# Kernel optimization log

Measured on AMD Instinct MI355X. Metric: run time of the kernel, lower is better.

The kernel has to match this reference:

```python
import jax, jax.numpy as jnp
import numpy as np

IN_SIZE = 1024
HIDDEN = 1024
BATCH = 4096


def _linear_params(key, out_dim, in_dim):
    # torch nn.Linear init: U(-1/sqrt(in_dim), 1/sqrt(in_dim)) for W and b
    k1, k2 = jax.random.split(key)
    bound = 1.0 / np.sqrt(in_dim)
    W = jax.random.uniform(k1, (out_dim, in_dim), jnp.float32, -bound, bound)
    b = jax.random.uniform(k2, (out_dim,), jnp.float32, -bound, bound)
    return W, b


def setup_inputs() -> dict:
    key = jax.random.key(0)
    keys = jax.random.split(key, 11)
    x = jax.random.normal(keys[0], (BATCH, IN_SIZE), jnp.float32)
    hidden = jax.random.normal(keys[1], (BATCH, HIDDEN), jnp.float32)
    cell = jax.random.normal(keys[2], (BATCH, HIDDEN), jnp.float32)
    names = ['xf', 'xi', 'xo', 'xc', 'hf', 'hi', 'ho', 'hc']
    inp = {'x': x, 'hidden': hidden, 'cell': cell}
    for n, k in zip(names, keys[3:]):
        in_dim = IN_SIZE if n[0] == 'x' else HIDDEN
        W, b = _linear_params(k, HIDDEN, in_dim)
        inp['W_' + n] = W
        inp['b_' + n] = b
    return inp


def reference(x, hidden, cell,
              W_xf, b_xf, W_xi, b_xi, W_xo, b_xo, W_xc, b_xc,
              W_hf, b_hf, W_hi, b_hi, W_ho, b_ho, W_hc, b_hc):
    # gates: sigmoid/tanh over (x-linear + h-linear) pairs
    f = jax.nn.sigmoid(x @ W_xf.T + b_xf + hidden @ W_hf.T + b_hf)
    i = jax.nn.sigmoid(x @ W_xi.T + b_xi + hidden @ W_hi.T + b_hi)
    o = jax.nn.sigmoid(x @ W_xo.T + b_xo + hidden @ W_ho.T + b_ho)
    c = jnp.tanh(x @ W_xc.T + b_xc + hidden @ W_hc.T + b_hc)
    updated_cell = f * cell + i * c
    updated_hidden = o * jnp.tanh(updated_cell)
    return updated_hidden, updated_cell
```

## Files before the change

### kernel.cpp

```cpp
#include <hip/hip_runtime.h>
#include <hip/hip_bf16.h>

#define BATCH 4096
#define NH    1024
#define KCAT  2048
#define NJ    4096
#define NT    (KCAT / 64)

typedef __bf16 bf16x8 __attribute__((ext_vector_type(8)));
typedef float  f32x4  __attribute__((ext_vector_type(4)));
typedef unsigned short u16x8 __attribute__((ext_vector_type(8)));

struct WPtrs { const float* wx[4]; const float* wh[4]; };
struct BPtrs { const float* bx[4]; const float* bh[4]; };

__device__ __forceinline__ unsigned short f2b(float f) {
  union { float f; unsigned u; } v; v.f = f;
  return (unsigned short)((v.u + 0x7fffu + ((v.u >> 16) & 1u)) >> 16);
}

__device__ __forceinline__ void gload_lds16(const void* g, void* l) {
  __builtin_amdgcn_global_load_lds(
      (const __attribute__((address_space(1))) unsigned int*)g,
      (__attribute__((address_space(3))) unsigned int*)l, 16, 0, 0);
}

__device__ __forceinline__ float sigmoid_f(float x) {
  x = fminf(fmaxf(x, -30.f), 30.f);
  return 1.f / (1.f + __expf(-x));
}
__device__ __forceinline__ float tanh_f(float x) {
  x = fminf(fmaxf(x, -15.f), 15.f);
  float e = __expf(2.f * x);
  return (e - 1.f) / (e + 1.f);
}

__global__ __launch_bounds__(256) void pack_all(
    const float* __restrict__ x, const float* __restrict__ h,
    WPtrs W, BPtrs B,
    __hip_bfloat16* __restrict__ Acat, __hip_bfloat16* __restrict__ Bcat,
    float* __restrict__ biasc) {
  int bid = blockIdx.x;
  if (bid < 4096) {
    int t = bid * 256 + threadIdx.x;
    int base = t * 8;
    int row = base >> 11;
    int k   = base & 2047;
    const float* src = (k < 1024) ? (x + (size_t)row * 1024 + k)
                                  : (h + (size_t)row * 1024 + (k - 1024));
    float4 v0 = ((const float4*)src)[0];
    float4 v1 = ((const float4*)src)[1];
    u16x8 o;
    o[0]=f2b(v0.x); o[1]=f2b(v0.y); o[2]=f2b(v0.z); o[3]=f2b(v0.w);
    o[4]=f2b(v1.x); o[5]=f2b(v1.y); o[6]=f2b(v1.z); o[7]=f2b(v1.w);
    *(u16x8*)((unsigned short*)Acat + base) = o;
  } else if (bid < 8192) {
    int t = (bid - 4096) * 256 + threadIdx.x;
    int base = t * 8;
    int j = base >> 11;
    int k = base & 2047;
    int n = ((j >> 6) << 4) + (j & 15);
    int g = (j >> 4) & 3;
    const float* src = (k < 1024) ? (W.wx[g] + (size_t)n * 1024 + k)
                                  : (W.wh[g] + (size_t)n * 1024 + (k - 1024));
    float4 v0 = ((const float4*)src)[0];
    float4 v1 = ((const float4*)src)[1];
    u16x8 o;
    o[0]=f2b(v0.x); o[1]=f2b(v0.y); o[2]=f2b(v0.z); o[3]=f2b(v0.w);
    o[4]=f2b(v1.x); o[5]=f2b(v1.y); o[6]=f2b(v1.z); o[7]=f2b(v1.w);
    *(u16x8*)((unsigned short*)Bcat + base) = o;
  } else {
    int i = (bid - 8192) * 256 + threadIdx.x;
    int g = i >> 10, n = i & 1023;
    biasc[i] = B.bx[g][n] + B.bh[g][n];
  }
}


#define STAGE_A_HALF(T, H)                                                      \
  {                                                                             \
    _Pragma("unroll")                                                           \
    for (int i_ = 0; i_ < 2; ++i_) {                                            \
      gload_lds16(Ag + (size_t)((H)*128 + i_*64 + strow) * KCAT + (T)*64 +      \
                      stchnk * 8,                                               \
                  &smem[((T)&1)*32768 + (H)*8192 + i_*4096 + w*512]);           \
    }                                                                           \
  }
#define STAGE_B_HALF(T, H)                                                      \
  {                                                                             \
    _Pragma("unroll")                                                           \
    for (int i_ = 0; i_ < 2; ++i_) {                                            \
      gload_lds16(Bg + (size_t)((H)*128 + i_*64 + strow) * KCAT + (T)*64 +      \
                      stchnk * 8,                                               \
                  &smem[((T)&1)*32768 + 16384 + (H)*8192 + i_*4096 + w*512]);   \
    }                                                                           \
  }

#define READ_A(BUFO, MQ)                                                        \
  {                                                                             \
    _Pragma("unroll")                                                           \
    for (int mf_ = 0; mf_ < 4; ++mf_) {                                         \
      af[mf_][0] = *(const bf16x8*)(smc + (BUFO) + arow0 +                      \
                                    ((MQ)*4 + mf_)*2048 + colb0);               \
      af[mf_][1] = *(const bf16x8*)(smc + (BUFO) + arow0 +                      \
                                    ((MQ)*4 + mf_)*2048 + colb1);               \
    }                                                                           \
  }
#define READ_B(BUFO, NQ, DST)                                                   \
  {                                                                             \
    _Pragma("unroll")                                                           \
    for (int nf_ = 0; nf_ < 2; ++nf_) {                                         \
      DST[nf_][0] = *(const bf16x8*)(smc + (BUFO) + brow0 +                     \
                                     ((NQ)*2 + nf_)*2048 + colb0);              \
      DST[nf_][1] = *(const bf16x8*)(smc + (BUFO) + brow0 +                     \
                                     ((NQ)*2 + nf_)*2048 + colb1);              \
    }                                                                           \
  }
#define MFMA_Q(MQ, NQ, BSET)                                                    \
  {                                                                             \
    _Pragma("unroll")                                                           \
    for (int ks_ = 0; ks_ < 2; ++ks_)                                           \
      _Pragma("unroll")                                                         \
      for (int mf_ = 0; mf_ < 4; ++mf_)                                         \
        _Pragma("unroll")                                                       \
        for (int nf_ = 0; nf_ < 2; ++nf_)                                       \
          acc[(MQ)*4 + mf_][(NQ)*2 + nf_] =                                     \
              __builtin_amdgcn_mfma_f32_16x16x32_bf16(                          \
                  af[mf_][ks_], BSET[nf_][ks_],                                 \
                  acc[(MQ)*4 + mf_][(NQ)*2 + nf_], 0, 0, 0);                    \
  }

#define BAR    __builtin_amdgcn_s_barrier()
#define PRIO1  __builtin_amdgcn_s_setprio(1)
#define PRIO0  __builtin_amdgcn_s_setprio(0)

__global__ __launch_bounds__(512, 2) void lstm_gemm8(
    const unsigned short* __restrict__ Acat,
    const unsigned short* __restrict__ Bcat,
    const float* __restrict__ biasc,
    const float* __restrict__ cell,
    float* __restrict__ outH, float* __restrict__ outC) {
  __shared__ unsigned short smem[65536];

  const int tid  = threadIdx.x;
  const int w    = tid >> 6;
  const int lane = tid & 63;
  const int wr   = w >> 2;
  const int wc   = w & 3;
  const int lr   = lane & 15;
  const int cb0  = ((lane >> 4) & 3) * 16;
  const int sx   = (lr & 7) << 4;

  const int bid = blockIdx.x;
  const int s   = (bid & 7) * 32 + (bid >> 3);
  const int bx  = s & 15;
  const int by  = s >> 4;

  const unsigned short* Ag = Acat + (size_t)(by * 256) * KCAT;
  const unsigned short* Bg = Bcat + (size_t)(bx * 256) * KCAT;

  const int strow  = w * 8 + (lane >> 3);
  const int stchnk = (lane & 7) ^ ((lane >> 3) & 7);

  const int arow0 = (wr * 128 + lr) * 128;
  const int brow0 = 32768 + (wc * 64 + lr) * 128;
  const int colb0 = cb0 ^ sx;
  const int colb1 = (64 + cb0) ^ sx;
  const char* smc = (const char*)smem;

  f32x4 acc[8][4] = {};
  bf16x8 af[4][2];
  bf16x8 bfr0[2][2];
  bf16x8 bfr1[2][2];

  STAGE_A_HALF(0, 0);
  STAGE_A_HALF(0, 1);
  STAGE_B_HALF(0, 0);
  STAGE_B_HALF(0, 1);
  STAGE_B_HALF(1, 0);
  STAGE_B_HALF(1, 1);
  asm volatile("s_waitcnt vmcnt(4)" ::: "memory");
  BAR;
  READ_A(0, 0);
  READ_B(0, 0, bfr0);

  for (int t = 0; t < NT; ++t) {
    const int curo = (t & 1) * 65536;
    const int nxto = curo ^ 65536;
    const bool s1 = (t + 1 < NT);
    const bool s2 = (t + 2 < NT);

    BAR;
    if (s1) STAGE_A_HALF(t + 1, 0);
    PRIO1; MFMA_Q(0, 0, bfr0); PRIO0;
    READ_B(curo, 1, bfr1);
    BAR;
    if (s1) STAGE_A_HALF(t + 1, 1);
    PRIO1; MFMA_Q(0, 1, bfr1); PRIO0;
    READ_A(curo, 1);
    BAR;
    if (s2) STAGE_B_HALF(t + 2, 0);
    PRIO1; MFMA_Q(1, 0, bfr0); PRIO0;
    if (s2) {
      STAGE_B_HALF(t + 2, 1);
      asm volatile("s_waitcnt vmcnt(4)" ::: "memory");
    } else if (s1) {
      asm volatile("s_waitcnt vmcnt(0)" ::: "memory");
    }
    BAR;
    PRIO1; MFMA_Q(1, 1, bfr1); PRIO0;
    if (s1) {
      READ_A(nxto, 0);
      READ_B(nxto, 0, bfr0);
    }
  }

  const int n_out = (bx * 4 + wc) * 16 + lr;
  const float bfv = biasc[n_out];
  const float biv = biasc[1024 + n_out];
  const float bov = biasc[2048 + n_out];
  const float bcv = biasc[3072 + n_out];
  const int q0 = (lane >> 4) * 4;

#pragma unroll
  for (int m = 0; m < 8; ++m) {
    int row0 = by * 256 + wr * 128 + m * 16 + q0;
#pragma unroll
    for (int q = 0; q < 4; ++q) {
      int row = row0 + q;
      float pf = acc[m][0][q] + bfv;
      float pi = acc[m][1][q] + biv;
      float po = acc[m][2][q] + bov;
      float pc = acc[m][3][q] + bcv;
      float fg = sigmoid_f(pf);
      float ig = sigmoid_f(pi);
      float og = sigmoid_f(po);
      float cg = tanh_f(pc);
      float cold = cell[(size_t)row * NH + n_out];
      float cn = fg * cold + ig * cg;
      float hn = og * tanh_f(cn);
      outH[(size_t)row * NH + n_out] = hn;
      outC[(size_t)row * NH + n_out] = cn;
    }
  }
}

extern "C" void kernel_launch(void* const* d_in, const int* in_sizes, int n_in,
                              void* d_out, int out_size, void* d_ws, size_t ws_size,
                              hipStream_t stream) {
  const float* x    = (const float*)d_in[0];
  const float* h    = (const float*)d_in[1];
  const float* cell = (const float*)d_in[2];
  WPtrs wp; BPtrs bp;
  for (int g = 0; g < 4; ++g) {
    wp.wx[g] = (const float*)d_in[3 + 2 * g];
    bp.bx[g] = (const float*)d_in[4 + 2 * g];
    wp.wh[g] = (const float*)d_in[11 + 2 * g];
    bp.bh[g] = (const float*)d_in[12 + 2 * g];
  }

  char* ws = (char*)d_ws;
  __hip_bfloat16* Acat = (__hip_bfloat16*)ws;
  __hip_bfloat16* Bcat = (__hip_bfloat16*)(ws + (size_t)BATCH * KCAT * 2);
  float* biasc = (float*)(ws + (size_t)BATCH * KCAT * 2 + (size_t)NJ * KCAT * 2);

  float* outH = (float*)d_out;
  float* outC = outH + (size_t)BATCH * NH;

  pack_all<<<8208, 256, 0, stream>>>(x, h, wp, bp, Acat, Bcat, biasc);

  lstm_gemm8<<<256, 512, 0, stream>>>((const unsigned short*)Acat,
                                      (const unsigned short*)Bcat,
                                      biasc, cell, outH, outC);
}
```

Baseline: 84.33 us.

## Prefetch cell state during GEMM and stage epilogue outputs through LDS

The old cell values are now loaded into registers during the second-to-last K iteration, so their global latency hides behind the last MFMA work instead of stalling the epilogue. The h and c results are written into swizzled LDS, then read back and stored as 16-byte vectors covering contiguous 64-column row segments, replacing scattered 4-byte stores. This adds 32 registers per thread for the prefetched cell values, two block barriers, and LDS traffic, which may raise register pressure.

```diff
diff --git a/kernel.cpp b/kernel.cpp
--- a/kernel.cpp
+++ b/kernel.cpp
@@ -168,10 +168,14 @@
   const int colb1 = (64 + cb0) ^ sx;
   const char* smc = (const char*)smem;
 
+  const int n_out = (bx * 4 + wc) * 16 + lr;
+  const int q0 = (lane >> 4) * 4;
+
   f32x4 acc[8][4] = {};
   bf16x8 af[4][2];
   bf16x8 bfr0[2][2];
   bf16x8 bfr1[2][2];
+  float cr[8][4];
 
   STAGE_A_HALF(0, 0);
   STAGE_A_HALF(0, 1);
@@ -213,21 +217,30 @@
       READ_A(nxto, 0);
       READ_B(nxto, 0, bfr0);
     }
-  }
-
-  const int n_out = (bx * 4 + wc) * 16 + lr;
+    if (t == NT - 2) {
+#pragma unroll
+      for (int m_ = 0; m_ < 8; ++m_)
+#pragma unroll
+        for (int q_ = 0; q_ < 4; ++q_) {
+          int row_ = by * 256 + wr * 128 + m_ * 16 + q0 + q_;
+          cr[m_][q_] = cell[(size_t)row_ * NH + n_out];
+        }
+    }
+  }
+
   const float bfv = biasc[n_out];
   const float biv = biasc[1024 + n_out];
   const float bov = biasc[2048 + n_out];
   const float bcv = biasc[3072 + n_out];
-  const int q0 = (lane >> 4) * 4;
-
+
+  __syncthreads();
+  float* lds_f = (float*)smem;
+
+  const int chunk = wc * 4 + (lr >> 2);
 #pragma unroll
   for (int m = 0; m < 8; ++m) {
-    int row0 = by * 256 + wr * 128 + m * 16 + q0;
 #pragma unroll
     for (int q = 0; q < 4; ++q) {
-      int row = row0 + q;
       float pf = acc[m][0][q] + bfv;
       float pi = acc[m][1][q] + biv;
       float po = acc[m][2][q] + bov;
@@ -236,12 +249,26 @@
       float ig = sigmoid_f(pi);
       float og = sigmoid_f(po);
       float cg = tanh_f(pc);
-      float cold = cell[(size_t)row * NH + n_out];
-      float cn = fg * cold + ig * cg;
+      float cn = fg * cr[m][q] + ig * cg;
       float hn = og * tanh_f(cn);
-      outH[(size_t)row * NH + n_out] = hn;
-      outC[(size_t)row * NH + n_out] = cn;
+      int row_l = wr * 128 + m * 16 + q0 + q;
+      int slot  = chunk ^ ((q0 + q) & 15);
+      int idx   = row_l * 64 + slot * 4 + (lr & 3);
+      lds_f[idx]         = hn;
+      lds_f[16384 + idx] = cn;
     }
+  }
+  __syncthreads();
+
+#pragma unroll
+  for (int i = 0; i < 8; ++i) {
+    int row_l = w * 32 + i * 4 + (lane >> 4);
+    int slotr = (lane & 15) ^ (row_l & 15);
+    f32x4 vH = *(const f32x4*)&lds_f[row_l * 64 + slotr * 4];
+    f32x4 vC = *(const f32x4*)&lds_f[16384 + row_l * 64 + slotr * 4];
+    size_t gaddr = (size_t)(by * 256 + row_l) * NH + bx * 64 + (lane & 15) * 4;
+    *(f32x4*)&outH[gaddr] = vH;
+    *(f32x4*)&outC[gaddr] = vC;
   }
 }
 
```

New measurement: 94.37 us. +11.9%, slower.

## Switch GEMM to 32x32x16 MFMA with 64x128 warp tiles and regrouped weights

Applied to the files above, without the earlier changes.

Replaces the 16x16x32 bf16 MFMA tiling (128x64 per wave) with 32x32x16 MFMA on a 2x4 wave grid of 64x128 tiles, and regroups the weight packing so each 32-column group holds one gate. The LDS read schedule is reorganised per k-slice, and the prologue/pipeline now prefetches A instead of B one tile ahead. The aim is fewer LDS fragment reads per FLOP and higher MFMA throughput. The cost is a different LDS access pattern that may cause bank conflicts under the existing swizzle, and changed register pressure.

```diff
diff --git a/kernel.cpp b/kernel.cpp
--- a/kernel.cpp
+++ b/kernel.cpp
@@ -8,7 +8,7 @@
 #define NT    (KCAT / 64)
 
 typedef __bf16 bf16x8 __attribute__((ext_vector_type(8)));
-typedef float  f32x4  __attribute__((ext_vector_type(4)));
+typedef float  f32x16 __attribute__((ext_vector_type(16)));
 typedef unsigned short u16x8 __attribute__((ext_vector_type(8)));
 
 struct WPtrs { const float* wx[4]; const float* wh[4]; };
@@ -59,8 +59,8 @@
     int base = t * 8;
     int j = base >> 11;
     int k = base & 2047;
-    int n = ((j >> 6) << 4) + (j & 15);
-    int g = (j >> 4) & 3;
+    int n = ((j >> 7) << 5) + (j & 31);
+    int g = (j >> 5) & 3;
     const float* src = (k < 1024) ? (W.wx[g] + (size_t)n * 1024 + k)
                                   : (W.wh[g] + (size_t)n * 1024 + (k - 1024));
     float4 v0 = ((const float4*)src)[0];
@@ -96,38 +96,27 @@
     }                                                                           \
   }
 
-#define READ_A(BUFO, MQ)                                                        \
-  {                                                                             \
-    _Pragma("unroll")                                                           \
-    for (int mf_ = 0; mf_ < 4; ++mf_) {                                         \
-      af[mf_][0] = *(const bf16x8*)(smc + (BUFO) + arow0 +                      \
-                                    ((MQ)*4 + mf_)*2048 + colb0);               \
-      af[mf_][1] = *(const bf16x8*)(smc + (BUFO) + arow0 +                      \
-                                    ((MQ)*4 + mf_)*2048 + colb1);               \
-    }                                                                           \
-  }
-#define READ_B(BUFO, NQ, DST)                                                   \
-  {                                                                             \
-    _Pragma("unroll")                                                           \
-    for (int nf_ = 0; nf_ < 2; ++nf_) {                                         \
-      DST[nf_][0] = *(const bf16x8*)(smc + (BUFO) + brow0 +                     \
-                                     ((NQ)*2 + nf_)*2048 + colb0);              \
-      DST[nf_][1] = *(const bf16x8*)(smc + (BUFO) + brow0 +                     \
-                                     ((NQ)*2 + nf_)*2048 + colb1);              \
-    }                                                                           \
-  }
-#define MFMA_Q(MQ, NQ, BSET)                                                    \
-  {                                                                             \
-    _Pragma("unroll")                                                           \
-    for (int ks_ = 0; ks_ < 2; ++ks_)                                           \
+#define CHB(KS) ((((KS)*2 + klh) << 4) ^ sxa)
+
+#define READ_AK(BUFO, KS)                                                       \
+  {                                                                             \
+    afk[KS][0] = *(const bf16x8*)(smc + (BUFO) + arow0 + CHB(KS));              \
+    afk[KS][1] = *(const bf16x8*)(smc + (BUFO) + arow0 + 4096 + CHB(KS));       \
+  }
+#define READ_BK(BUFO, KS, DST)                                                  \
+  {                                                                             \
+    _Pragma("unroll")                                                           \
+    for (int nt_ = 0; nt_ < 4; ++nt_)                                           \
+      DST[nt_] = *(const bf16x8*)(smc + (BUFO) + brow0 + nt_*4096 + CHB(KS));   \
+  }
+#define MFMA_K(KS, BSET)                                                        \
+  {                                                                             \
+    _Pragma("unroll")                                                           \
+    for (int mt_ = 0; mt_ < 2; ++mt_)                                           \
       _Pragma("unroll")                                                         \
-      for (int mf_ = 0; mf_ < 4; ++mf_)                                         \
-        _Pragma("unroll")                                                       \
-        for (int nf_ = 0; nf_ < 2; ++nf_)                                       \
-          acc[(MQ)*4 + mf_][(NQ)*2 + nf_] =                                     \
-              __builtin_amdgcn_mfma_f32_16x16x32_bf16(                          \
-                  af[mf_][ks_], BSET[nf_][ks_],                                 \
-                  acc[(MQ)*4 + mf_][(NQ)*2 + nf_], 0, 0, 0);                    \
+      for (int nt_ = 0; nt_ < 4; ++nt_)                                         \
+        acc[mt_][nt_] = __builtin_amdgcn_mfma_f32_32x32x16_bf16(                \
+            afk[KS][mt_], BSET[nt_], acc[mt_][nt_], 0, 0, 0);                   \
   }
 
 #define BAR    __builtin_amdgcn_s_barrier()
@@ -145,11 +134,11 @@
   const int tid  = threadIdx.x;
   const int w    = tid >> 6;
   const int lane = tid & 63;
-  const int wr   = w >> 2;
-  const int wc   = w & 3;
-  const int lr   = lane & 15;
-  const int cb0  = ((lane >> 4) & 3) * 16;
-  const int sx   = (lr & 7) << 4;
+  const int wr   = w >> 1;
+  const int wc   = w & 1;
+  const int l31  = lane & 31;
+  const int klh  = lane >> 5;
+  const int sxa  = (lane & 7) << 4;
 
   const int bid = blockIdx.x;
   const int s   = (bid & 7) * 32 + (bid >> 3);
@@ -162,27 +151,25 @@
   const int strow  = w * 8 + (lane >> 3);
   const int stchnk = (lane & 7) ^ ((lane >> 3) & 7);
 
-  const int arow0 = (wr * 128 + lr) * 128;
-  const int brow0 = 32768 + (wc * 64 + lr) * 128;
-  const int colb0 = cb0 ^ sx;
-  const int colb1 = (64 + cb0) ^ sx;
+  const int arow0 = (wr * 64 + l31) * 128;
+  const int brow0 = 32768 + (wc * 128 + l31) * 128;
   const char* smc = (const char*)smem;
 
-  f32x4 acc[8][4] = {};
-  bf16x8 af[4][2];
-  bf16x8 bfr0[2][2];
-  bf16x8 bfr1[2][2];
+  f32x16 acc[2][4] = {};
+  bf16x8 afk[4][2];
+  bf16x8 bf0[4];
+  bf16x8 bf1[4];
 
   STAGE_A_HALF(0, 0);
   STAGE_A_HALF(0, 1);
   STAGE_B_HALF(0, 0);
   STAGE_B_HALF(0, 1);
-  STAGE_B_HALF(1, 0);
-  STAGE_B_HALF(1, 1);
+  STAGE_A_HALF(1, 0);
+  STAGE_A_HALF(1, 1);
   asm volatile("s_waitcnt vmcnt(4)" ::: "memory");
   BAR;
-  READ_A(0, 0);
-  READ_B(0, 0, bfr0);
+  READ_AK(0, 0);
+  READ_BK(0, 0, bf0);
 
   for (int t = 0; t < NT; ++t) {
     const int curo = (t & 1) * 65536;
@@ -191,56 +178,59 @@
     const bool s2 = (t + 2 < NT);
 
     BAR;
-    if (s1) STAGE_A_HALF(t + 1, 0);
-    PRIO1; MFMA_Q(0, 0, bfr0); PRIO0;
-    READ_B(curo, 1, bfr1);
-    BAR;
-    if (s1) STAGE_A_HALF(t + 1, 1);
-    PRIO1; MFMA_Q(0, 1, bfr1); PRIO0;
-    READ_A(curo, 1);
-    BAR;
-    if (s2) STAGE_B_HALF(t + 2, 0);
-    PRIO1; MFMA_Q(1, 0, bfr0); PRIO0;
+    if (s1) STAGE_B_HALF(t + 1, 0);
+    PRIO1; MFMA_K(0, bf0); PRIO0;
+    READ_AK(curo, 1);
+    READ_BK(curo, 1, bf1);
+    READ_AK(curo, 2);
+    READ_AK(curo, 3);
+    BAR;
+    if (s1) STAGE_B_HALF(t + 1, 1);
+    PRIO1; MFMA_K(1, bf1); PRIO0;
+    READ_BK(curo, 2, bf0);
+    BAR;
+    if (s2) STAGE_A_HALF(t + 2, 0);
+    PRIO1; MFMA_K(2, bf0); PRIO0;
+    READ_BK(curo, 3, bf1);
     if (s2) {
-      STAGE_B_HALF(t + 2, 1);
+      STAGE_A_HALF(t + 2, 1);
       asm volatile("s_waitcnt vmcnt(4)" ::: "memory");
     } else if (s1) {
       asm volatile("s_waitcnt vmcnt(0)" ::: "memory");
     }
     BAR;
-    PRIO1; MFMA_Q(1, 1, bfr1); PRIO0;
+    PRIO1; MFMA_K(3, bf1); PRIO0;
     if (s1) {
-      READ_A(nxto, 0);
-      READ_B(nxto, 0, bfr0);
+      READ_AK(nxto, 0);
+      READ_BK(nxto, 0, bf0);
     }
   }
 
-  const int n_out = (bx * 4 + wc) * 16 + lr;
-  const float bfv = biasc[n_out];
-  const float biv = biasc[1024 + n_out];
-  const float bov = biasc[2048 + n_out];
-  const float bcv = biasc[3072 + n_out];
-  const int q0 = (lane >> 4) * 4;
+  const int nbase = (bx * 2 + wc) * 32 + l31;
+  const float bfv = biasc[nbase];
+  const float biv = biasc[1024 + nbase];
+  const float bov = biasc[2048 + nbase];
+  const float bcv = biasc[3072 + nbase];
+  const int rbase = by * 256 + wr * 64 + 4 * klh;
 
 #pragma unroll
-  for (int m = 0; m < 8; ++m) {
-    int row0 = by * 256 + wr * 128 + m * 16 + q0;
+  for (int mt = 0; mt < 2; ++mt) {
 #pragma unroll
-    for (int q = 0; q < 4; ++q) {
-      int row = row0 + q;
-      float pf = acc[m][0][q] + bfv;
-      float pi = acc[m][1][q] + biv;
-      float po = acc[m][2][q] + bov;
-      float pc = acc[m][3][q] + bcv;
+    for (int r = 0; r < 16; ++r) {
+      int row = rbase + mt * 32 + (r & 3) + 8 * (r >> 2);
+      float pf = acc[mt][0][r] + bfv;
+      float pi = acc[mt][1][r] + biv;
+      float po = acc[mt][2][r] + bov;
+      float pc = acc[mt][3][r] + bcv;
       float fg = sigmoid_f(pf);
       float ig = sigmoid_f(pi);
       float og = sigmoid_f(po);
       float cg = tanh_f(pc);
-      float cold = cell[(size_t)row * NH + n_out];
+      float cold = cell[(size_t)row * NH + nbase];
       float cn = fg * cold + ig * cg;
       float hn = og * tanh_f(cn);
-      outH[(size_t)row * NH + n_out] = hn;
-      outC[(size_t)row * NH + n_out] = cn;
+      outH[(size_t)row * NH + nbase] = hn;
+      outC[(size_t)row * NH + nbase] = cn;
     }
   }
 }
```

New measurement: 91.20 us. 8.2% more time.

## Restructure main loop into two M-halves with full B fragments per phase

Applied to the files above, without the earlier changes.

Replaces the four-phase loop, which alternated two half-sets of B fragments with A quarters, by a two-phase loop. Each phase loads all four B fragments and runs 32 MFMAs per M-half. This halves the barriers per K-tile and issues the A and B staging in larger batches, cutting sync overhead. In exchange it uses more B fragment registers at the same time and gives less fine-grained overlap between LDS reads and MFMAs, which may hurt occupancy at 2 waves per SIMD or leave LDS latency exposed.

```diff
diff --git a/kernel.cpp b/kernel.cpp
--- a/kernel.cpp
+++ b/kernel.cpp
@@ -106,28 +106,28 @@
                                     ((MQ)*4 + mf_)*2048 + colb1);               \
     }                                                                           \
   }
-#define READ_B(BUFO, NQ, DST)                                                   \
-  {                                                                             \
-    _Pragma("unroll")                                                           \
-    for (int nf_ = 0; nf_ < 2; ++nf_) {                                         \
-      DST[nf_][0] = *(const bf16x8*)(smc + (BUFO) + brow0 +                     \
-                                     ((NQ)*2 + nf_)*2048 + colb0);              \
-      DST[nf_][1] = *(const bf16x8*)(smc + (BUFO) + brow0 +                     \
-                                     ((NQ)*2 + nf_)*2048 + colb1);              \
-    }                                                                           \
-  }
-#define MFMA_Q(MQ, NQ, BSET)                                                    \
+#define READ_B_ALL(BUFO)                                                        \
+  {                                                                             \
+    _Pragma("unroll")                                                           \
+    for (int nf_ = 0; nf_ < 4; ++nf_) {                                         \
+      bfr[nf_][0] = *(const bf16x8*)(smc + (BUFO) + brow0 +                     \
+                                     nf_*2048 + colb0);                         \
+      bfr[nf_][1] = *(const bf16x8*)(smc + (BUFO) + brow0 +                     \
+                                     nf_*2048 + colb1);                         \
+    }                                                                           \
+  }
+#define MFMA_MQ(MQ)                                                             \
   {                                                                             \
     _Pragma("unroll")                                                           \
     for (int ks_ = 0; ks_ < 2; ++ks_)                                           \
       _Pragma("unroll")                                                         \
       for (int mf_ = 0; mf_ < 4; ++mf_)                                         \
         _Pragma("unroll")                                                       \
-        for (int nf_ = 0; nf_ < 2; ++nf_)                                       \
-          acc[(MQ)*4 + mf_][(NQ)*2 + nf_] =                                     \
+        for (int nf_ = 0; nf_ < 4; ++nf_)                                       \
+          acc[(MQ)*4 + mf_][nf_] =                                              \
               __builtin_amdgcn_mfma_f32_16x16x32_bf16(                          \
-                  af[mf_][ks_], BSET[nf_][ks_],                                 \
-                  acc[(MQ)*4 + mf_][(NQ)*2 + nf_], 0, 0, 0);                    \
+                  af[mf_][ks_], bfr[nf_][ks_],                                  \
+                  acc[(MQ)*4 + mf_][nf_], 0, 0, 0);                             \
   }
 
 #define BAR    __builtin_amdgcn_s_barrier()
@@ -170,8 +170,7 @@
 
   f32x4 acc[8][4] = {};
   bf16x8 af[4][2];
-  bf16x8 bfr0[2][2];
-  bf16x8 bfr1[2][2];
+  bf16x8 bfr[4][2];
 
   STAGE_A_HALF(0, 0);
   STAGE_A_HALF(0, 1);
@@ -182,7 +181,7 @@
   asm volatile("s_waitcnt vmcnt(4)" ::: "memory");
   BAR;
   READ_A(0, 0);
-  READ_B(0, 0, bfr0);
+  READ_B_ALL(0);
 
   for (int t = 0; t < NT; ++t) {
     const int curo = (t & 1) * 65536;
@@ -191,27 +190,21 @@
     const bool s2 = (t + 2 < NT);
 
     BAR;
-    if (s1) STAGE_A_HALF(t + 1, 0);
-    PRIO1; MFMA_Q(0, 0, bfr0); PRIO0;
-    READ_B(curo, 1, bfr1);
-    BAR;
-    if (s1) STAGE_A_HALF(t + 1, 1);
-    PRIO1; MFMA_Q(0, 1, bfr1); PRIO0;
+    if (s1) { STAGE_A_HALF(t + 1, 0); STAGE_A_HALF(t + 1, 1); }
+    PRIO1; MFMA_MQ(0); PRIO0;
     READ_A(curo, 1);
-    BAR;
-    if (s2) STAGE_B_HALF(t + 2, 0);
-    PRIO1; MFMA_Q(1, 0, bfr0); PRIO0;
     if (s2) {
+      STAGE_B_HALF(t + 2, 0);
       STAGE_B_HALF(t + 2, 1);
       asm volatile("s_waitcnt vmcnt(4)" ::: "memory");
     } else if (s1) {
       asm volatile("s_waitcnt vmcnt(0)" ::: "memory");
     }
     BAR;
-    PRIO1; MFMA_Q(1, 1, bfr1); PRIO0;
+    PRIO1; MFMA_MQ(1); PRIO0;
     if (s1) {
       READ_A(nxto, 0);
-      READ_B(nxto, 0, bfr0);
+      READ_B_ALL(nxto);
     }
   }
 
```

Result: no change. 85.41 us (+1.3%).
